# Kernel optimization log

Hardware: AMD Instinct MI355X
Metric: run time of the kernel (lower is better)

## Reference

```python
import jax, jax.numpy as jnp
import numpy as np


def setup_inputs() -> dict:
    key = jax.random.key(0)
    k_u, k_a, k_b, k_c, k_d = jax.random.split(key, 5)
    B, T, Din, Dout, S = 16, 4096, 256, 256, 256
    return {
        "u": jax.random.normal(k_u, (B, T, Din), dtype=jnp.float32),
        "a_raw": jnp.zeros((S,), dtype=jnp.float32),
        "b": jax.random.normal(k_b, (S, Din), dtype=jnp.float32) * 0.1,
        "c": jax.random.normal(k_c, (Dout, S), dtype=jnp.float32) * 0.1,
        "d": jax.random.normal(k_d, (Dout, Din), dtype=jnp.float32) * 0.1,
    }


def reference(u, a_raw, b, c, d):
    # u: (B, T, Din) -> y: (B, T, Dout)
    # Recurrence: x_t = a * x_{t-1} + b @ u_t ;  y_t = c @ x_t + d @ u_t
    a = jnp.tanh(a_raw)                                  # (S,)
    Bu = jnp.einsum('btd,sd->bts', u, b)                 # input projection, (B,T,S)

    def step(x, bu_t):
        x = x * a + bu_t                                 # diagonal state update
        return x, x

    x0 = jnp.zeros((u.shape[0], a.shape[0]), dtype=u.dtype)
    _, xs = jax.lax.scan(step, x0, jnp.swapaxes(Bu, 0, 1))  # xs: (T,B,S)
    xs = jnp.swapaxes(xs, 0, 1)                              # (B,T,S)

    y = jnp.einsum('bts,os->bto', xs, c) + jnp.einsum('bti,oi->bto', u, d)
    return y  # dropout(p=0.0) is identity
```

## Files before the change

kernel.cpp:

```cpp
#include <hip/hip_runtime.h>

#define DEV __device__ __forceinline__

typedef unsigned short u16;
typedef __attribute__((ext_vector_type(8))) __bf16 bf16x8;
typedef __attribute__((ext_vector_type(4))) float f32x4;
typedef __attribute__((ext_vector_type(8))) unsigned short u16x8;
typedef __attribute__((ext_vector_type(4))) unsigned short u16x4;

static constexpr int NB = 16;
static constexpr int NT = 4096;
static constexpr int NCH = 64;
static constexpr int LCH = 64;

DEV u16 f2bf(float f) {
  unsigned u = __builtin_bit_cast(unsigned, f);
  u += 0x7fffu + ((u >> 16) & 1u);
  return (u16)(u >> 16);
}
DEV float bf2f(u16 h) {
  unsigned u = ((unsigned)h) << 16;
  return __builtin_bit_cast(float, u);
}

DEV void gl_lds16(const void* gp, void* lp) {
  __builtin_amdgcn_global_load_lds(
      (__attribute__((address_space(1))) void*)(void*)gp,
      (__attribute__((address_space(3))) void*)lp, 16, 0, 0);
}

__global__ __launch_bounds__(256) void prep_k(const float* __restrict__ a_raw,
                                              const float* __restrict__ b,
                                              const float* __restrict__ c,
                                              const float* __restrict__ d,
                                              float* __restrict__ af,
                                              u16* __restrict__ bw,
                                              u16* __restrict__ cw,
                                              u16* __restrict__ dw) {
  int i = blockIdx.x * 256 + threadIdx.x;
  if (i < 256) af[i] = tanhf(a_raw[i]);
  bw[i] = f2bf(b[i]);
  cw[i] = f2bf(c[i]);
  dw[i] = f2bf(d[i]);
}

__global__ __launch_bounds__(256) void convu_k(const float* __restrict__ u,
                                               u16* __restrict__ ub) {
  size_t i = ((size_t)blockIdx.x * 256 + threadIdx.x) * 8;
  float4 v0 = *reinterpret_cast<const float4*>(u + i);
  float4 v1 = *reinterpret_cast<const float4*>(u + i + 4);
  u16x8 o;
  o[0] = f2bf(v0.x); o[1] = f2bf(v0.y); o[2] = f2bf(v0.z); o[3] = f2bf(v0.w);
  o[4] = f2bf(v1.x); o[5] = f2bf(v1.y); o[6] = f2bf(v1.z); o[7] = f2bf(v1.w);
  *reinterpret_cast<u16x8*>(ub + i) = o;
}

__global__ __launch_bounds__(256) void gemm1_k(const u16* __restrict__ ubf,
                                               const u16* __restrict__ bw,
                                               const float* __restrict__ af,
                                               u16* __restrict__ bu,
                                               float* __restrict__ carry) {
  __shared__ u16 As[128 * 64];
  __shared__ u16 Bs[128 * 64];
  const int tid = threadIdx.x;
  const int lane = tid & 63;
  const int wid = tid >> 6;
  const int wm = wid >> 1, wn = wid & 1;
  const int panel = blockIdx.x;
  const size_t row0 = (size_t)blockIdx.y * 128;
  const int col0 = panel * 128;

  const int rstg = tid >> 3;
  const int c16 = tid & 7;

  const f32x4 zero = {0.f, 0.f, 0.f, 0.f};
  f32x4 acc[4][4];
#pragma unroll
  for (int i = 0; i < 4; ++i)
#pragma unroll
    for (int j = 0; j < 4; ++j) acc[i][j] = zero;

#pragma unroll
  for (int kt = 0; kt < 4; ++kt) {
    const int kb = kt * 64;
#pragma unroll
    for (int j = 0; j < 4; ++j) {
      int row = j * 32 + rstg;
      int sc = c16 ^ (row & 7);
      gl_lds16(ubf + (row0 + row) * 256 + kb + sc * 8,
               (char*)As + j * 4096 + wid * 1024);
      gl_lds16(bw + (size_t)(col0 + row) * 256 + kb + sc * 8,
               (char*)Bs + j * 4096 + wid * 1024);
    }
    __syncthreads();
#pragma unroll
    for (int kk = 0; kk < 2; ++kk) {
      const int ks = kk * 4 + (lane >> 4);
      bf16x8 afr[4], bfr[4];
#pragma unroll
      for (int mi = 0; mi < 4; ++mi) {
        int ar = wm * 64 + mi * 16 + (lane & 15);
        afr[mi] = *reinterpret_cast<const bf16x8*>(&As[ar * 64 + (ks ^ (ar & 7)) * 8]);
      }
#pragma unroll
      for (int ni = 0; ni < 4; ++ni) {
        int br = wn * 64 + ni * 16 + (lane & 15);
        bfr[ni] = *reinterpret_cast<const bf16x8*>(&Bs[br * 64 + (ks ^ (br & 7)) * 8]);
      }
#pragma unroll
      for (int mi = 0; mi < 4; ++mi)
#pragma unroll
        for (int ni = 0; ni < 4; ++ni)
          acc[mi][ni] = __builtin_amdgcn_mfma_f32_16x16x32_bf16(
              afr[mi], bfr[ni], acc[mi][ni], 0, 0, 0);
    }
    if (kt < 3) __syncthreads();
  }

#pragma unroll
  for (int mi = 0; mi < 4; ++mi) {
    int rl = wm * 64 + mi * 16 + (lane >> 4) * 4;
#pragma unroll
    for (int ni = 0; ni < 4; ++ni) {
      int col = col0 + wn * 64 + ni * 16 + (lane & 15);
#pragma unroll
      for (int q = 0; q < 4; ++q) {
        size_t R = row0 + rl + q;
        bu[R * 256 + (((col >> 3) ^ ((int)R & 7)) * 8) + (col & 7)] = f2bf(acc[mi][ni][q]);
      }
    }
  }

  {
    const int chunk = (int)(blockIdx.y) * 2 + wm;
    const int tb = (lane >> 4) * 4;
#pragma unroll
    for (int ni = 0; ni < 4; ++ni) {
      int col = col0 + wn * 64 + ni * 16 + (lane & 15);
      float a = af[col];
      float c2 = a * a, c4 = c2 * c2, c8 = c4 * c4;
      float a12 = c8 * c4;
      float a13 = a12 * a;
      float base = (tb == 0) ? a12 : (tb == 4) ? c8 : (tb == 8) ? c4 : 1.0f;
      float p = base, s = 0.f;
#pragma unroll
      for (int mi = 3; mi >= 0; --mi) {
#pragma unroll
        for (int q = 3; q >= 0; --q) {
          s = fmaf(p, acc[mi][ni][q], s);
          if (q) p *= a;
        }
        if (mi) p *= a13;
      }
      s += __shfl_xor(s, 16, 64);
      s += __shfl_xor(s, 32, 64);
      if ((lane >> 4) == 0) carry[(size_t)chunk * 256 + col] = s;
    }
  }
}

__global__ __launch_bounds__(256) void scan2_k(const float* __restrict__ carry,
                                               const float* __restrict__ af,
                                               float* __restrict__ initb) {
  int b = blockIdx.x;
  int s = threadIdx.x;
  float a = af[s];
  float aL = a;
#pragma unroll
  for (int i = 0; i < 6; ++i) aL *= aL;
  float x = 0.f;
  for (int k = 0; k < NCH; ++k) {
    size_t idx = ((size_t)(b * NCH + k)) * 256 + s;
    float cv = carry[idx];
    initb[idx] = x;
    x = fmaf(aL, x, cv);
  }
}

__global__ __launch_bounds__(512, 4) void gemm2_k(const u16* __restrict__ bu,
                                                  const u16* __restrict__ cw,
                                                  const u16* __restrict__ dw,
                                                  const u16* __restrict__ ubf,
                                                  const float* __restrict__ af,
                                                  const float* __restrict__ initb,
                                                  float* __restrict__ y) {
  __shared__ u16 XS[128 * 256];
  __shared__ u16 CS[128 * 64];
  const int tid = threadIdx.x;
  const int lane = tid & 63;
  const int wid = tid >> 6;
  const int wr = wid >> 2, wc = wid & 3;
  const int bx = blockIdx.y;
  const int col0 = blockIdx.x * 128;

  const char* src = (const char*)bu + (size_t)bx * 65536;
#pragma unroll
  for (int j = 0; j < 8; ++j)
    gl_lds16(src + j * 8192 + tid * 16, (char*)XS + j * 8192 + wid * 1024);
#pragma unroll
  for (int r = 0; r < 2; ++r) {
    int brow = r * 64 + (tid >> 3);
    int sc = (tid & 7) ^ (brow & 7);
    gl_lds16(cw + (size_t)(col0 + brow) * 256 + 0 + sc * 8,
             (char*)CS + r * 8192 + wid * 1024);
  }
  __syncthreads();

  {
    const int hf = tid >> 8;
    const int s = tid & 255;
    const float a = af[s];
    float x = initb[(size_t)(bx * 2 + hf) * 256 + s];
    const int r0 = hf * 64;
    const int slot = s >> 3;
    const int off = (s & 7);
#pragma unroll 8
    for (int t = 0; t < 64; ++t) {
      int r = r0 + t;
      int bi = r * 256 + ((slot ^ (r & 7)) * 8) + off;
      x = fmaf(a, x, bf2f(XS[bi]));
      XS[bi] = f2bf(x);
    }
  }

  f32x4 acc[4][2];
  const f32x4 zero = {0.f, 0.f, 0.f, 0.f};
#pragma unroll
  for (int mi = 0; mi < 4; ++mi) { acc[mi][0] = zero; acc[mi][1] = zero; }
  __syncthreads();

#pragma unroll
  for (int kt = 0; kt < 4; ++kt) {
#pragma unroll
    for (int kk = 0; kk < 2; ++kk) {
      const int ksl = kk * 4 + (lane >> 4);
      const int ksg = kt * 8 + ksl;
      bf16x8 afr[4], bfr[2];
#pragma unroll
      for (int mi = 0; mi < 4; ++mi) {
        int ar = wr * 64 + mi * 16 + (lane & 15);
        afr[mi] = *reinterpret_cast<const bf16x8*>(&XS[ar * 256 + ((ksg ^ (ar & 7)) * 8)]);
      }
#pragma unroll
      for (int ni = 0; ni < 2; ++ni) {
        int nr = wc * 32 + ni * 16 + (lane & 15);
        bfr[ni] = *reinterpret_cast<const bf16x8*>(&CS[nr * 64 + ((ksl ^ (nr & 7)) * 8)]);
      }
#pragma unroll
      for (int mi = 0; mi < 4; ++mi)
#pragma unroll
        for (int ni = 0; ni < 2; ++ni)
          acc[mi][ni] = __builtin_amdgcn_mfma_f32_16x16x32_bf16(
              afr[mi], bfr[ni], acc[mi][ni], 0, 0, 0);
    }
    if (kt < 3) {
      __syncthreads();
#pragma unroll
      for (int r = 0; r < 2; ++r) {
        int brow = r * 64 + (tid >> 3);
        int sc = (tid & 7) ^ (brow & 7);
        gl_lds16(cw + (size_t)(col0 + brow) * 256 + (kt + 1) * 64 + sc * 8,
                 (char*)CS + r * 8192 + wid * 1024);
      }
      __syncthreads();
    }
  }

#pragma unroll
  for (int kt = 0; kt < 4; ++kt) {
    __syncthreads();
#pragma unroll
    for (int j = 0; j < 2; ++j) {
      int row = j * 64 + (tid >> 3);
      int sc = (tid & 7) ^ (row & 7);
      gl_lds16(ubf + ((size_t)bx * 128 + row) * 256 + kt * 64 + sc * 8,
               (char*)XS + j * 8192 + wid * 1024);
    }
#pragma unroll
    for (int r = 0; r < 2; ++r) {
      int brow = r * 64 + (tid >> 3);
      int sc = (tid & 7) ^ (brow & 7);
      gl_lds16(dw + (size_t)(col0 + brow) * 256 + kt * 64 + sc * 8,
               (char*)CS + r * 8192 + wid * 1024);
    }
    __syncthreads();
#pragma unroll
    for (int kk = 0; kk < 2; ++kk) {
      const int ksl = kk * 4 + (lane >> 4);
      bf16x8 afr[4], bfr[2];
#pragma unroll
      for (int mi = 0; mi < 4; ++mi) {
        int ar = wr * 64 + mi * 16 + (lane & 15);
        afr[mi] = *reinterpret_cast<const bf16x8*>(
            (const char*)XS + ar * 128 + ((ksl ^ (ar & 7)) * 16));
      }
#pragma unroll
      for (int ni = 0; ni < 2; ++ni) {
        int nr = wc * 32 + ni * 16 + (lane & 15);
        bfr[ni] = *reinterpret_cast<const bf16x8*>(&CS[nr * 64 + ((ksl ^ (nr & 7)) * 8)]);
      }
#pragma unroll
      for (int mi = 0; mi < 4; ++mi)
#pragma unroll
        for (int ni = 0; ni < 2; ++ni)
          acc[mi][ni] = __builtin_amdgcn_mfma_f32_16x16x32_bf16(
              afr[mi], bfr[ni], acc[mi][ni], 0, 0, 0);
    }
  }

#pragma unroll
  for (int mi = 0; mi < 4; ++mi) {
    int rlb = wr * 64 + mi * 16 + (lane >> 4) * 4;
#pragma unroll
    for (int ni = 0; ni < 2; ++ni) {
      int col = col0 + wc * 32 + ni * 16 + (lane & 15);
#pragma unroll
      for (int q = 0; q < 4; ++q)
        y[(size_t)(bx * 128 + rlb + q) * 256 + col] = acc[mi][ni][q];
    }
  }
}

extern "C" void kernel_launch(void* const* d_in, const int* in_sizes, int n_in,
                              void* d_out, int out_size, void* d_ws, size_t ws_size,
                              hipStream_t stream) {
  const float* u = (const float*)d_in[0];
  const float* a_raw = (const float*)d_in[1];
  const float* b = (const float*)d_in[2];
  const float* c = (const float*)d_in[3];
  const float* d = (const float*)d_in[4];
  float* y = (float*)d_out;
  char* ws = (char*)d_ws;

  const size_t MB = 1u << 20;
  float* af = (float*)(ws);
  u16* bw = (u16*)(ws + 4096);
  u16* cw = (u16*)(ws + 4096 + 131072);
  u16* dw = (u16*)(ws + 4096 + 2 * 131072);
  u16* ubf = (u16*)(ws + 1 * MB);
  u16* bu = (u16*)(ws + 33 * MB);
  float* carry = (float*)(ws + 65 * MB);
  float* initb = (float*)(ws + 66 * MB);

  prep_k<<<256, 256, 0, stream>>>(a_raw, b, c, d, af, bw, cw, dw);
  convu_k<<<8192, 256, 0, stream>>>(u, ubf);
  gemm1_k<<<dim3(2, 512), 256, 0, stream>>>(ubf, bw, af, bu, carry);
  scan2_k<<<16, 256, 0, stream>>>(carry, af, initb);
  gemm2_k<<<dim3(2, 512), 512, 0, stream>>>(bu, cw, dw, ubf, af, initb, y);
}
```

Before: 93.03 us.

## Shrink scan chunks to 16 rows and halve gemm2 tile to 64 rows

Gemm1 now writes per-16-row carries and lays out Bu in K-panel-major swizzled tiles. The carry scan runs over 1024 sub-chunks with a16 decay. Gemm2 uses 64-row tiles with 2048 blocks. Each thread scans two independent 16-row chains with register batching, and the C and D GEMM loops merge into one pipelined loop that reuses the XS buffer for u panels. This raises occupancy (launch bounds 6) and shortens the serial in-kernel scan, at the cost of a longer carry scan and reloading weights twice as often.

```diff
diff --git a/kernel.cpp b/kernel.cpp
--- a/kernel.cpp
+++ b/kernel.cpp
@@ -6,12 +6,8 @@
 typedef __attribute__((ext_vector_type(8))) __bf16 bf16x8;
 typedef __attribute__((ext_vector_type(4))) float f32x4;
 typedef __attribute__((ext_vector_type(8))) unsigned short u16x8;
-typedef __attribute__((ext_vector_type(4))) unsigned short u16x4;
-
-static constexpr int NB = 16;
-static constexpr int NT = 4096;
-static constexpr int NCH = 64;
-static constexpr int LCH = 64;
+
+static constexpr int NCH_TOT = 1024;
 
 DEV u16 f2bf(float f) {
   unsigned u = __builtin_bit_cast(unsigned, f);
@@ -59,7 +55,7 @@
                                                const u16* __restrict__ bw,
                                                const float* __restrict__ af,
                                                u16* __restrict__ bu,
-                                               float* __restrict__ carry) {
+                                               float* __restrict__ carry4) {
   __shared__ u16 As[128 * 64];
   __shared__ u16 Bs[128 * 64];
   const int tid = threadIdx.x;
@@ -117,129 +113,147 @@
     if (kt < 3) __syncthreads();
   }
 
+  const size_t t2 = (size_t)blockIdx.y * 2 + wm;
 #pragma unroll
   for (int mi = 0; mi < 4; ++mi) {
-    int rl = wm * 64 + mi * 16 + (lane >> 4) * 4;
+    int rbase = mi * 16 + (lane >> 4) * 4;
 #pragma unroll
     for (int ni = 0; ni < 4; ++ni) {
       int col = col0 + wn * 64 + ni * 16 + (lane & 15);
+      int colpart = (col >> 6) * 4096 + (col & 7);
+      int sl = (col >> 3) & 7;
 #pragma unroll
       for (int q = 0; q < 4; ++q) {
-        size_t R = row0 + rl + q;
-        bu[R * 256 + (((col >> 3) ^ ((int)R & 7)) * 8) + (col & 7)] = f2bf(acc[mi][ni][q]);
+        int r = rbase + q;
+        bu[t2 * 16384 + colpart + r * 64 + ((sl ^ (r & 7)) * 8)] = f2bf(acc[mi][ni][q]);
       }
     }
   }
 
   {
-    const int chunk = (int)(blockIdx.y) * 2 + wm;
     const int tb = (lane >> 4) * 4;
 #pragma unroll
     for (int ni = 0; ni < 4; ++ni) {
       int col = col0 + wn * 64 + ni * 16 + (lane & 15);
       float a = af[col];
-      float c2 = a * a, c4 = c2 * c2, c8 = c4 * c4;
-      float a12 = c8 * c4;
-      float a13 = a12 * a;
+      float c2 = a * a, c4 = c2 * c2, c8 = c4 * c4, a12 = c8 * c4;
       float base = (tb == 0) ? a12 : (tb == 4) ? c8 : (tb == 8) ? c4 : 1.0f;
-      float p = base, s = 0.f;
-#pragma unroll
-      for (int mi = 3; mi >= 0; --mi) {
+#pragma unroll
+      for (int mi = 0; mi < 4; ++mi) {
+        float p = base, sq = 0.f;
 #pragma unroll
         for (int q = 3; q >= 0; --q) {
-          s = fmaf(p, acc[mi][ni][q], s);
+          sq = fmaf(p, acc[mi][ni][q], sq);
           if (q) p *= a;
         }
-        if (mi) p *= a13;
-      }
-      s += __shfl_xor(s, 16, 64);
-      s += __shfl_xor(s, 32, 64);
-      if ((lane >> 4) == 0) carry[(size_t)chunk * 256 + col] = s;
-    }
-  }
-}
-
-__global__ __launch_bounds__(256) void scan2_k(const float* __restrict__ carry,
+        sq += __shfl_xor(sq, 16, 64);
+        sq += __shfl_xor(sq, 32, 64);
+        if ((lane >> 4) == 0) carry4[t2 * 1024 + mi * 256 + col] = sq;
+      }
+    }
+  }
+}
+
+__global__ __launch_bounds__(256) void scan2_k(const float* __restrict__ carry4,
                                                const float* __restrict__ af,
-                                               float* __restrict__ initb) {
+                                               float* __restrict__ initb4) {
   int b = blockIdx.x;
   int s = threadIdx.x;
   float a = af[s];
-  float aL = a;
-#pragma unroll
-  for (int i = 0; i < 6; ++i) aL *= aL;
+  float a16 = a * a; a16 = a16 * a16; a16 = a16 * a16; a16 = a16 * a16;
   float x = 0.f;
-  for (int k = 0; k < NCH; ++k) {
-    size_t idx = ((size_t)(b * NCH + k)) * 256 + s;
-    float cv = carry[idx];
-    initb[idx] = x;
-    x = fmaf(aL, x, cv);
-  }
-}
-
-__global__ __launch_bounds__(512, 4) void gemm2_k(const u16* __restrict__ bu,
+  size_t base = (size_t)b * 64 * 1024 + s;
+  float c0 = carry4[base], c1 = carry4[base + 256],
+        c2 = carry4[base + 512], c3 = carry4[base + 768];
+  for (int k = 0; k < 64; ++k) {
+    size_t idx = base + (size_t)k * 1024;
+    float n0 = 0.f, n1 = 0.f, n2 = 0.f, n3 = 0.f;
+    if (k < 63) {
+      size_t nx = idx + 1024;
+      n0 = carry4[nx]; n1 = carry4[nx + 256]; n2 = carry4[nx + 512]; n3 = carry4[nx + 768];
+    }
+    initb4[idx] = x;        x = fmaf(a16, x, c0);
+    initb4[idx + 256] = x;  x = fmaf(a16, x, c1);
+    initb4[idx + 512] = x;  x = fmaf(a16, x, c2);
+    initb4[idx + 768] = x;  x = fmaf(a16, x, c3);
+    c0 = n0; c1 = n1; c2 = n2; c3 = n3;
+  }
+}
+
+__global__ __launch_bounds__(512, 6) void gemm2_k(const u16* __restrict__ bu,
                                                   const u16* __restrict__ cw,
                                                   const u16* __restrict__ dw,
                                                   const u16* __restrict__ ubf,
                                                   const float* __restrict__ af,
-                                                  const float* __restrict__ initb,
+                                                  const float* __restrict__ initb4,
                                                   float* __restrict__ y) {
-  __shared__ u16 XS[128 * 256];
+  __shared__ u16 XS[64 * 256];
   __shared__ u16 CS[128 * 64];
   const int tid = threadIdx.x;
   const int lane = tid & 63;
   const int wid = tid >> 6;
   const int wr = wid >> 2, wc = wid & 3;
-  const int bx = blockIdx.y;
+  const int by = blockIdx.y;
   const int col0 = blockIdx.x * 128;
 
-  const char* src = (const char*)bu + (size_t)bx * 65536;
-#pragma unroll
-  for (int j = 0; j < 8; ++j)
+  const char* src = (const char*)bu + (size_t)by * 32768;
+#pragma unroll
+  for (int j = 0; j < 4; ++j)
     gl_lds16(src + j * 8192 + tid * 16, (char*)XS + j * 8192 + wid * 1024);
 #pragma unroll
-  for (int r = 0; r < 2; ++r) {
-    int brow = r * 64 + (tid >> 3);
+  for (int rr = 0; rr < 2; ++rr) {
+    int brow = rr * 64 + (tid >> 3);
     int sc = (tid & 7) ^ (brow & 7);
-    gl_lds16(cw + (size_t)(col0 + brow) * 256 + 0 + sc * 8,
-             (char*)CS + r * 8192 + wid * 1024);
+    gl_lds16(cw + (size_t)(col0 + brow) * 256 + sc * 8,
+             (char*)CS + rr * 8192 + wid * 1024);
   }
   __syncthreads();
 
   {
-    const int hf = tid >> 8;
     const int s = tid & 255;
+    const int pair = tid >> 8;
     const float a = af[s];
-    float x = initb[(size_t)(bx * 2 + hf) * 256 + s];
-    const int r0 = hf * 64;
-    const int slot = s >> 3;
-    const int off = (s & 7);
-#pragma unroll 8
-    for (int t = 0; t < 64; ++t) {
-      int r = r0 + t;
-      int bi = r * 256 + ((slot ^ (r & 7)) * 8) + off;
-      x = fmaf(a, x, bf2f(XS[bi]));
-      XS[bi] = f2bf(x);
-    }
-  }
-
-  f32x4 acc[4][2];
+    const int colpart = (s >> 6) * 4096 + (s & 7);
+    const int sl = (s >> 3) & 7;
+    float x1 = initb4[(size_t)by * 1024 + (pair * 2) * 256 + s];
+    float x2 = initb4[(size_t)by * 1024 + (pair * 2 + 1) * 256 + s];
+    const int rA0 = pair * 32, rB0 = pair * 32 + 16;
+    float vA[16], vB[16];
+#pragma unroll
+    for (int t = 0; t < 16; ++t) {
+      int rA = rA0 + t, rB = rB0 + t;
+      vA[t] = bf2f(XS[colpart + rA * 64 + ((sl ^ (rA & 7)) * 8)]);
+      vB[t] = bf2f(XS[colpart + rB * 64 + ((sl ^ (rB & 7)) * 8)]);
+    }
+#pragma unroll
+    for (int t = 0; t < 16; ++t) {
+      x1 = fmaf(a, x1, vA[t]); vA[t] = x1;
+      x2 = fmaf(a, x2, vB[t]); vB[t] = x2;
+    }
+#pragma unroll
+    for (int t = 0; t < 16; ++t) {
+      int rA = rA0 + t, rB = rB0 + t;
+      XS[colpart + rA * 64 + ((sl ^ (rA & 7)) * 8)] = f2bf(vA[t]);
+      XS[colpart + rB * 64 + ((sl ^ (rB & 7)) * 8)] = f2bf(vB[t]);
+    }
+  }
+  __syncthreads();
+
+  f32x4 acc[2][2];
   const f32x4 zero = {0.f, 0.f, 0.f, 0.f};
-#pragma unroll
-  for (int mi = 0; mi < 4; ++mi) { acc[mi][0] = zero; acc[mi][1] = zero; }
-  __syncthreads();
-
-#pragma unroll
-  for (int kt = 0; kt < 4; ++kt) {
+  acc[0][0] = zero; acc[0][1] = zero; acc[1][0] = zero; acc[1][1] = zero;
+
+#pragma unroll
+  for (int kt8 = 0; kt8 < 8; ++kt8) {
 #pragma unroll
     for (int kk = 0; kk < 2; ++kk) {
       const int ksl = kk * 4 + (lane >> 4);
-      const int ksg = kt * 8 + ksl;
-      bf16x8 afr[4], bfr[2];
-#pragma unroll
-      for (int mi = 0; mi < 4; ++mi) {
-        int ar = wr * 64 + mi * 16 + (lane & 15);
-        afr[mi] = *reinterpret_cast<const bf16x8*>(&XS[ar * 256 + ((ksg ^ (ar & 7)) * 8)]);
+      bf16x8 afr[2], bfr[2];
+#pragma unroll
+      for (int mi = 0; mi < 2; ++mi) {
+        int ar = wr * 32 + mi * 16 + (lane & 15);
+        afr[mi] = *reinterpret_cast<const bf16x8*>(
+            &XS[(kt8 & 3) * 4096 + ar * 64 + ((ksl ^ (ar & 7)) * 8)]);
       }
 #pragma unroll
       for (int ni = 0; ni < 2; ++ni) {
@@ -247,76 +261,41 @@
         bfr[ni] = *reinterpret_cast<const bf16x8*>(&CS[nr * 64 + ((ksl ^ (nr & 7)) * 8)]);
       }
 #pragma unroll
-      for (int mi = 0; mi < 4; ++mi)
+      for (int mi = 0; mi < 2; ++mi)
 #pragma unroll
         for (int ni = 0; ni < 2; ++ni)
           acc[mi][ni] = __builtin_amdgcn_mfma_f32_16x16x32_bf16(
               afr[mi], bfr[ni], acc[mi][ni], 0, 0, 0);
     }
-    if (kt < 3) {
+    if (kt8 < 7) {
       __syncthreads();
-#pragma unroll
-      for (int r = 0; r < 2; ++r) {
-        int brow = r * 64 + (tid >> 3);
+      if (kt8 < 4) {
+        int r = tid >> 3, cs = tid & 7;
+        gl_lds16(ubf + ((size_t)by * 64 + r) * 256 + kt8 * 64 + ((cs ^ (r & 7)) * 8),
+                 (char*)XS + kt8 * 8192 + wid * 1024);
+      }
+      const u16* Wn = (kt8 < 3) ? cw : dw;
+      const int kb = (kt8 < 3) ? (kt8 + 1) * 64 : (kt8 - 3) * 64;
+#pragma unroll
+      for (int rr = 0; rr < 2; ++rr) {
+        int brow = rr * 64 + (tid >> 3);
         int sc = (tid & 7) ^ (brow & 7);
-        gl_lds16(cw + (size_t)(col0 + brow) * 256 + (kt + 1) * 64 + sc * 8,
-                 (char*)CS + r * 8192 + wid * 1024);
+        gl_lds16(Wn + (size_t)(col0 + brow) * 256 + kb + sc * 8,
+                 (char*)CS + rr * 8192 + wid * 1024);
       }
       __syncthreads();
     }
   }
 
 #pragma unroll
-  for (int kt = 0; kt < 4; ++kt) {
-    __syncthreads();
-#pragma unroll
-    for (int j = 0; j < 2; ++j) {
-      int row = j * 64 + (tid >> 3);
-      int sc = (tid & 7) ^ (row & 7);
-      gl_lds16(ubf + ((size_t)bx * 128 + row) * 256 + kt * 64 + sc * 8,
-               (char*)XS + j * 8192 + wid * 1024);
-    }
-#pragma unroll
-    for (int r = 0; r < 2; ++r) {
-      int brow = r * 64 + (tid >> 3);
-      int sc = (tid & 7) ^ (brow & 7);
-      gl_lds16(dw + (size_t)(col0 + brow) * 256 + kt * 64 + sc * 8,
-               (char*)CS + r * 8192 + wid * 1024);
-    }
-    __syncthreads();
-#pragma unroll
-    for (int kk = 0; kk < 2; ++kk) {
-      const int ksl = kk * 4 + (lane >> 4);
-      bf16x8 afr[4], bfr[2];
-#pragma unroll
-      for (int mi = 0; mi < 4; ++mi) {
-        int ar = wr * 64 + mi * 16 + (lane & 15);
-        afr[mi] = *reinterpret_cast<const bf16x8*>(
-            (const char*)XS + ar * 128 + ((ksl ^ (ar & 7)) * 16));
-      }
-#pragma unroll
-      for (int ni = 0; ni < 2; ++ni) {
-        int nr = wc * 32 + ni * 16 + (lane & 15);
-        bfr[ni] = *reinterpret_cast<const bf16x8*>(&CS[nr * 64 + ((ksl ^ (nr & 7)) * 8)]);
-      }
-#pragma unroll
-      for (int mi = 0; mi < 4; ++mi)
-#pragma unroll
-        for (int ni = 0; ni < 2; ++ni)
-          acc[mi][ni] = __builtin_amdgcn_mfma_f32_16x16x32_bf16(
-              afr[mi], bfr[ni], acc[mi][ni], 0, 0, 0);
-    }
-  }
-
-#pragma unroll
-  for (int mi = 0; mi < 4; ++mi) {
-    int rlb = wr * 64 + mi * 16 + (lane >> 4) * 4;
+  for (int mi = 0; mi < 2; ++mi) {
+    int rlb = wr * 32 + mi * 16 + (lane >> 4) * 4;
 #pragma unroll
     for (int ni = 0; ni < 2; ++ni) {
       int col = col0 + wc * 32 + ni * 16 + (lane & 15);
 #pragma unroll
       for (int q = 0; q < 4; ++q)
-        y[(size_t)(bx * 128 + rlb + q) * 256 + col] = acc[mi][ni][q];
+        y[((size_t)by * 64 + rlb + q) * 256 + col] = acc[mi][ni][q];
     }
   }
 }
@@ -339,12 +318,12 @@
   u16* dw = (u16*)(ws + 4096 + 2 * 131072);
   u16* ubf = (u16*)(ws + 1 * MB);
   u16* bu = (u16*)(ws + 33 * MB);
-  float* carry = (float*)(ws + 65 * MB);
-  float* initb = (float*)(ws + 66 * MB);
+  float* carry4 = (float*)(ws + 65 * MB);
+  float* initb4 = (float*)(ws + 69 * MB);
 
   prep_k<<<256, 256, 0, stream>>>(a_raw, b, c, d, af, bw, cw, dw);
   convu_k<<<8192, 256, 0, stream>>>(u, ubf);
-  gemm1_k<<<dim3(2, 512), 256, 0, stream>>>(ubf, bw, af, bu, carry);
-  scan2_k<<<16, 256, 0, stream>>>(carry, af, initb);
-  gemm2_k<<<dim3(2, 512), 512, 0, stream>>>(bu, cw, dw, ubf, af, initb, y);
-}
+  gemm1_k<<<dim3(2, 512), 256, 0, stream>>>(ubf, bw, af, bu, carry4);
+  scan2_k<<<16, 256, 0, stream>>>(carry4, af, initb4);
+  gemm2_k<<<dim3(2, 1024), 512, 0, stream>>>(bu, cw, dw, ubf, af, initb4, y);
+}
```

After: 96.27 us. +3.5%, slower.

## Compute D·u in first GEMM and seed second GEMM accumulators with it

Applied to the files above, without the earlier changes.

The b and d weights are concatenated into one 512-row matrix so gemm1 computes both the B·u projection and the D·u skip term with 4 column panels. The D·u result is stored as bf16 and loaded as the initial accumulator in gemm2, which drops gemm2's second K-loop that re-streamed ubf and dw. This trades an extra 32MB bf16 write and read of the D·u result for fewer MFMA passes over ubf in gemm2. It also rounds the skip-term sum to bf16, and gemm2's grid is transposed so blocks sharing a row tile launch adjacently.

```diff
diff --git a/kernel.cpp b/kernel.cpp
--- a/kernel.cpp
+++ b/kernel.cpp
@@ -6,12 +6,6 @@
 typedef __attribute__((ext_vector_type(8))) __bf16 bf16x8;
 typedef __attribute__((ext_vector_type(4))) float f32x4;
 typedef __attribute__((ext_vector_type(8))) unsigned short u16x8;
-typedef __attribute__((ext_vector_type(4))) unsigned short u16x4;
-
-static constexpr int NB = 16;
-static constexpr int NT = 4096;
-static constexpr int NCH = 64;
-static constexpr int LCH = 64;
 
 DEV u16 f2bf(float f) {
   unsigned u = __builtin_bit_cast(unsigned, f);
@@ -34,14 +28,13 @@
                                               const float* __restrict__ c,
                                               const float* __restrict__ d,
                                               float* __restrict__ af,
-                                              u16* __restrict__ bw,
-                                              u16* __restrict__ cw,
-                                              u16* __restrict__ dw) {
+                                              u16* __restrict__ wq,
+                                              u16* __restrict__ cw) {
   int i = blockIdx.x * 256 + threadIdx.x;
   if (i < 256) af[i] = tanhf(a_raw[i]);
-  bw[i] = f2bf(b[i]);
+  wq[i] = f2bf(b[i]);
+  wq[65536 + i] = f2bf(d[i]);
   cw[i] = f2bf(c[i]);
-  dw[i] = f2bf(d[i]);
 }
 
 __global__ __launch_bounds__(256) void convu_k(const float* __restrict__ u,
@@ -56,9 +49,10 @@
 }
 
 __global__ __launch_bounds__(256) void gemm1_k(const u16* __restrict__ ubf,
-                                               const u16* __restrict__ bw,
+                                               const u16* __restrict__ wq,
                                                const float* __restrict__ af,
                                                u16* __restrict__ bu,
+                                               u16* __restrict__ ud,
                                                float* __restrict__ carry) {
   __shared__ u16 As[128 * 64];
   __shared__ u16 Bs[128 * 64];
@@ -89,7 +83,7 @@
       int sc = c16 ^ (row & 7);
       gl_lds16(ubf + (row0 + row) * 256 + kb + sc * 8,
                (char*)As + j * 4096 + wid * 1024);
-      gl_lds16(bw + (size_t)(col0 + row) * 256 + kb + sc * 8,
+      gl_lds16(wq + (size_t)(col0 + row) * 256 + kb + sc * 8,
                (char*)Bs + j * 4096 + wid * 1024);
     }
     __syncthreads();
@@ -117,21 +111,21 @@
     if (kt < 3) __syncthreads();
   }
 
-#pragma unroll
-  for (int mi = 0; mi < 4; ++mi) {
-    int rl = wm * 64 + mi * 16 + (lane >> 4) * 4;
-#pragma unroll
-    for (int ni = 0; ni < 4; ++ni) {
-      int col = col0 + wn * 64 + ni * 16 + (lane & 15);
-#pragma unroll
-      for (int q = 0; q < 4; ++q) {
-        size_t R = row0 + rl + q;
-        bu[R * 256 + (((col >> 3) ^ ((int)R & 7)) * 8) + (col & 7)] = f2bf(acc[mi][ni][q]);
-      }
-    }
-  }
-
-  {
+  if (panel < 2) {
+#pragma unroll
+    for (int mi = 0; mi < 4; ++mi) {
+      int rl = wm * 64 + mi * 16 + (lane >> 4) * 4;
+#pragma unroll
+      for (int ni = 0; ni < 4; ++ni) {
+        int col = col0 + wn * 64 + ni * 16 + (lane & 15);
+#pragma unroll
+        for (int q = 0; q < 4; ++q) {
+          size_t R = row0 + rl + q;
+          bu[R * 256 + (((col >> 3) ^ ((int)R & 7)) * 8) + (col & 7)] =
+              f2bf(acc[mi][ni][q]);
+        }
+      }
+    }
     const int chunk = (int)(blockIdx.y) * 2 + wm;
     const int tb = (lane >> 4) * 4;
 #pragma unroll
@@ -156,6 +150,20 @@
       s += __shfl_xor(s, 32, 64);
       if ((lane >> 4) == 0) carry[(size_t)chunk * 256 + col] = s;
     }
+  } else {
+#pragma unroll
+    for (int mi = 0; mi < 4; ++mi) {
+      int rl = wm * 64 + mi * 16 + (lane >> 4) * 4;
+#pragma unroll
+      for (int ni = 0; ni < 4; ++ni) {
+        int col = col0 + wn * 64 + ni * 16 + (lane & 15);
+#pragma unroll
+        for (int q = 0; q < 4; ++q) {
+          size_t R = row0 + rl + q;
+          ud[R * 256 + (col - 256)] = f2bf(acc[mi][ni][q]);
+        }
+      }
+    }
   }
 }
 
@@ -169,8 +177,8 @@
 #pragma unroll
   for (int i = 0; i < 6; ++i) aL *= aL;
   float x = 0.f;
-  for (int k = 0; k < NCH; ++k) {
-    size_t idx = ((size_t)(b * NCH + k)) * 256 + s;
+  for (int k = 0; k < 64; ++k) {
+    size_t idx = ((size_t)(b * 64 + k)) * 256 + s;
     float cv = carry[idx];
     initb[idx] = x;
     x = fmaf(aL, x, cv);
@@ -179,8 +187,7 @@
 
 __global__ __launch_bounds__(512, 4) void gemm2_k(const u16* __restrict__ bu,
                                                   const u16* __restrict__ cw,
-                                                  const u16* __restrict__ dw,
-                                                  const u16* __restrict__ ubf,
+                                                  const u16* __restrict__ ud,
                                                   const float* __restrict__ af,
                                                   const float* __restrict__ initb,
                                                   float* __restrict__ y) {
@@ -190,8 +197,8 @@
   const int lane = tid & 63;
   const int wid = tid >> 6;
   const int wr = wid >> 2, wc = wid & 3;
-  const int bx = blockIdx.y;
-  const int col0 = blockIdx.x * 128;
+  const int bx = blockIdx.x;
+  const int col0 = blockIdx.y * 128;
 
   const char* src = (const char*)bu + (size_t)bx * 65536;
 #pragma unroll
@@ -224,9 +231,17 @@
   }
 
   f32x4 acc[4][2];
-  const f32x4 zero = {0.f, 0.f, 0.f, 0.f};
-#pragma unroll
-  for (int mi = 0; mi < 4; ++mi) { acc[mi][0] = zero; acc[mi][1] = zero; }
+#pragma unroll
+  for (int mi = 0; mi < 4; ++mi) {
+    int rlb = wr * 64 + mi * 16 + (lane >> 4) * 4;
+#pragma unroll
+    for (int ni = 0; ni < 2; ++ni) {
+      int col = col0 + wc * 32 + ni * 16 + (lane & 15);
+#pragma unroll
+      for (int q = 0; q < 4; ++q)
+        acc[mi][ni][q] = bf2f(ud[(size_t)(bx * 128 + rlb + q) * 256 + col]);
+    }
+  }
   __syncthreads();
 
 #pragma unroll
@@ -263,48 +278,6 @@
                  (char*)CS + r * 8192 + wid * 1024);
       }
       __syncthreads();
-    }
-  }
-
-#pragma unroll
-  for (int kt = 0; kt < 4; ++kt) {
-    __syncthreads();
-#pragma unroll
-    for (int j = 0; j < 2; ++j) {
-      int row = j * 64 + (tid >> 3);
-      int sc = (tid & 7) ^ (row & 7);
-      gl_lds16(ubf + ((size_t)bx * 128 + row) * 256 + kt * 64 + sc * 8,
-               (char*)XS + j * 8192 + wid * 1024);
-    }
-#pragma unroll
-    for (int r = 0; r < 2; ++r) {
-      int brow = r * 64 + (tid >> 3);
-      int sc = (tid & 7) ^ (brow & 7);
-      gl_lds16(dw + (size_t)(col0 + brow) * 256 + kt * 64 + sc * 8,
-               (char*)CS + r * 8192 + wid * 1024);
-    }
-    __syncthreads();
-#pragma unroll
-    for (int kk = 0; kk < 2; ++kk) {
-      const int ksl = kk * 4 + (lane >> 4);
-      bf16x8 afr[4], bfr[2];
-#pragma unroll
-      for (int mi = 0; mi < 4; ++mi) {
-        int ar = wr * 64 + mi * 16 + (lane & 15);
-        afr[mi] = *reinterpret_cast<const bf16x8*>(
-            (const char*)XS + ar * 128 + ((ksl ^ (ar & 7)) * 16));
-      }
-#pragma unroll
-      for (int ni = 0; ni < 2; ++ni) {
-        int nr = wc * 32 + ni * 16 + (lane & 15);
-        bfr[ni] = *reinterpret_cast<const bf16x8*>(&CS[nr * 64 + ((ksl ^ (nr & 7)) * 8)]);
-      }
-#pragma unroll
-      for (int mi = 0; mi < 4; ++mi)
-#pragma unroll
-        for (int ni = 0; ni < 2; ++ni)
-          acc[mi][ni] = __builtin_amdgcn_mfma_f32_16x16x32_bf16(
-              afr[mi], bfr[ni], acc[mi][ni], 0, 0, 0);
     }
   }
 
@@ -334,17 +307,17 @@
 
   const size_t MB = 1u << 20;
   float* af = (float*)(ws);
-  u16* bw = (u16*)(ws + 4096);
-  u16* cw = (u16*)(ws + 4096 + 131072);
-  u16* dw = (u16*)(ws + 4096 + 2 * 131072);
+  u16* wq = (u16*)(ws + 4096);
+  u16* cw = (u16*)(ws + 4096 + 262144);
   u16* ubf = (u16*)(ws + 1 * MB);
   u16* bu = (u16*)(ws + 33 * MB);
   float* carry = (float*)(ws + 65 * MB);
   float* initb = (float*)(ws + 66 * MB);
-
-  prep_k<<<256, 256, 0, stream>>>(a_raw, b, c, d, af, bw, cw, dw);
+  u16* ud = (u16*)(ws + 67 * MB);
+
+  prep_k<<<256, 256, 0, stream>>>(a_raw, b, c, d, af, wq, cw);
   convu_k<<<8192, 256, 0, stream>>>(u, ubf);
-  gemm1_k<<<dim3(2, 512), 256, 0, stream>>>(ubf, bw, af, bu, carry);
+  gemm1_k<<<dim3(4, 512), 256, 0, stream>>>(ubf, wq, af, bu, ud, carry);
   scan2_k<<<16, 256, 0, stream>>>(carry, af, initb);
-  gemm2_k<<<dim3(2, 512), 512, 0, stream>>>(bu, cw, dw, ubf, af, initb, y);
-}
+  gemm2_k<<<dim3(512, 2), 512, 0, stream>>>(bu, cw, ud, af, initb, y);
+}
```

After: 118.2 us. +27.0%, slower.
